# Kernel tuning notes

Hardware: AMD Instinct MI355X
Metric: run time of the kernel (lower is better)

The kernel has to match this reference:

```python
import jax, jax.numpy as jnp
import numpy as np

EPS_LN = 1e-5
EPS_BN = 1e-5


def ln_channels(x, w, b):
    # LayerNorm2d: normalize over channel dim of NCHW
    mu = x.mean(axis=1, keepdims=True)
    var = x.var(axis=1, keepdims=True)
    return (x - mu) / jnp.sqrt(var + EPS_LN) * w[None, :, None, None] + b[None, :, None, None]


def bn_eval(x, g, b):
    # eval-mode BatchNorm2d with running_mean=0, running_var=1
    return x / jnp.sqrt(1.0 + EPS_BN) * g[None, :, None, None] + b[None, :, None, None]


def conv1x1(x, w, b):
    return jnp.einsum('bchw,oc->bohw', x, w) + b[None, :, None, None]


def q_shift(x):
    # directional shift: 4 channel quarters shifted right/left/down/up by 1 px (zero pad)
    C = x.shape[1]
    q = C // 4
    return jnp.concatenate([
        jnp.pad(x[:, 0 * q:1 * q, :, :-1], ((0, 0), (0, 0), (0, 0), (1, 0))),
        jnp.pad(x[:, 1 * q:2 * q, :, 1:], ((0, 0), (0, 0), (0, 0), (0, 1))),
        jnp.pad(x[:, 2 * q:3 * q, :-1, :], ((0, 0), (0, 0), (1, 0), (0, 0))),
        jnp.pad(x[:, 3 * q:4 * q, 1:, :], ((0, 0), (0, 0), (0, 1), (0, 0))),
    ], axis=1)


def wkv_scan(k, v, w_neg, u):
    # numerically-stable RWKV WKV recurrence. k, v: [N, T, C]; w_neg (negative decay), u: [C]
    N, T, C = k.shape

    def step(carry, kv):
        a, b, p = carry
        kt, vt = kv
        q = jnp.maximum(p, u + kt)
        e1 = jnp.exp(p - q)
        e2 = jnp.exp(u + kt - q)
        out = (e1 * a + e2 * vt) / (e1 * b + e2)
        q2 = jnp.maximum(p + w_neg, kt)
        f1 = jnp.exp(p + w_neg - q2)
        f2 = jnp.exp(kt - q2)
        return (f1 * a + f2 * vt, f1 * b + f2, q2), out

    init = (jnp.zeros((N, C), k.dtype), jnp.zeros((N, C), k.dtype), jnp.full((N, C), -1e38, k.dtype))
    _, outs = jax.lax.scan(step, init, (jnp.swapaxes(k, 0, 1), jnp.swapaxes(v, 0, 1)))
    return jnp.swapaxes(outs, 0, 1)


def shape_guided_rwkv(x, mask, mix_k, mix_v, mix_r, Wk, Wv, Wr, Wo, decay, first, kn_w, kn_b):
    B, C, H, W = x.shape
    xs = q_shift(x)
    x_sh = mask * xs + (1.0 - mask) * x  # saliency-guided shift blend
    mk = mix_k[None, :, None, None]
    mv = mix_v[None, :, None, None]
    mr = mix_r[None, :, None, None]
    xk = x * mk + x_sh * (1.0 - mk)
    xv = x * mv + x_sh * (1.0 - mv)
    xr = x * mr + x_sh * (1.0 - mr)
    k = jnp.einsum('bchw,oc->bohw', xk, Wk)
    v = jnp.einsum('bchw,oc->bohw', xv, Wv)
    sr = jax.nn.sigmoid(jnp.einsum('bchw,oc->bohw', xr, Wr))
    w_neg = -jnp.exp(decay)
    # horizontal orientation: scan each row left->right
    kh = k.transpose(0, 2, 3, 1).reshape(B * H, W, C)
    vh = v.transpose(0, 2, 3, 1).reshape(B * H, W, C)
    wkv_h = wkv_scan(kh, vh, w_neg, first).reshape(B, H, W, C).transpose(0, 3, 1, 2)
    # vertical orientation: scan each column top->bottom
    kv_ = k.transpose(0, 3, 2, 1).reshape(B * W, H, C)
    vv_ = v.transpose(0, 3, 2, 1).reshape(B * W, H, C)
    wkv_v = wkv_scan(kv_, vv_, w_neg, first).reshape(B, W, H, C).transpose(0, 3, 2, 1)
    wkv = 0.5 * (wkv_h + wkv_v)
    wkv = ln_channels(wkv, kn_w, kn_b)  # key_norm=True
    out = jnp.einsum('bchw,oc->bohw', sr * wkv, Wo)
    return x + out


def channel_fusion(x, c1_w, c1_b, bn1_g, bn1_b, c2_w, c2_b, bn2_g, bn2_b, c3_w, c3_b, bn3_g, bn3_b):
    # grouped 3x3 conv (groups=2) -> GELU -> BN -> 1x1 expand -> GELU -> BN -> 1x1 reduce -> GELU -> BN
    y = jax.lax.conv_general_dilated(x, c1_w, (1, 1), 'SAME',
                                     dimension_numbers=('NCHW', 'OIHW', 'NCHW'),
                                     feature_group_count=2) + c1_b[None, :, None, None]
    y = bn_eval(jax.nn.gelu(y, approximate=False), bn1_g, bn1_b)
    y = bn_eval(jax.nn.gelu(conv1x1(y, c2_w, c2_b), approximate=False), bn2_g, bn2_b)
    y = bn_eval(jax.nn.gelu(conv1x1(y, c3_w, c3_b), approximate=False), bn3_g, bn3_b)
    return y


def patch_expand(x, up_w, up_b, s=2):
    B, C, H, W = x.shape
    y = conv1x1(x, up_w, up_b)  # [B, Cout*s*s, H, W]
    Cout = y.shape[1] // (s * s)
    y = y.reshape(B, Cout, s, s, H, W).transpose(0, 1, 4, 2, 5, 3).reshape(B, Cout, H * s, W * s)
    return y


def setup_inputs() -> dict:
    key = jax.random.key(0)
    B, C, Cs, Cout, H, W, s = 8, 256, 512, 128, 64, 64, 2
    ks = jax.random.split(key, 32)
    sc = C ** -0.5
    inp = {
        'x': jax.random.normal(ks[0], (B, C, H, W), jnp.float32),
        'skip': jax.random.normal(ks[1], (B, Cs, H, W), jnp.float32),
        'saliency_mask': jax.random.uniform(ks[2], (B, 1, H, W), jnp.float32),
        'ln1_w': jnp.ones((C,)), 'ln1_b': jnp.zeros((C,)),
        'ln2_w': jnp.ones((C,)), 'ln2_b': jnp.zeros((C,)),
        'mix_k': jax.random.uniform(ks[3], (C,)),
        'mix_v': jax.random.uniform(ks[4], (C,)),
        'mix_r': jax.random.uniform(ks[5], (C,)),
        'Wk': jax.random.normal(ks[6], (C, C)) * sc,
        'Wv': jax.random.normal(ks[7], (C, C)) * sc,
        'Wr': jax.random.normal(ks[8], (C, C)) * sc,
        'Wo': jax.random.normal(ks[9], (C, C)) * sc,
        'decay': jax.random.normal(ks[10], (C,)) * 0.5,
        'first': jax.random.normal(ks[11], (C,)) * 0.5,
        'kn_w': jnp.ones((C,)), 'kn_b': jnp.zeros((C,)),
        'sp_w': jax.random.normal(ks[12], (C, Cs)) * (Cs ** -0.5),
        'sp_b': jnp.zeros((C,)),
        'c1_w': jax.random.normal(ks[13], (2 * C, C, 3, 3)) * ((C * 9) ** -0.5),
        'c1_b': jnp.zeros((2 * C,)),
        'bn1_g': jnp.ones((2 * C,)), 'bn1_b': jnp.zeros((2 * C,)),
        'c2_w': jax.random.normal(ks[14], (4 * C, 2 * C)) * ((2 * C) ** -0.5),
        'c2_b': jnp.zeros((4 * C,)),
        'bn2_g': jnp.ones((4 * C,)), 'bn2_b': jnp.zeros((4 * C,)),
        'c3_w': jax.random.normal(ks[15], (C, 4 * C)) * ((4 * C) ** -0.5),
        'c3_b': jnp.zeros((C,)),
        'bn3_g': jnp.ones((C,)), 'bn3_b': jnp.zeros((C,)),
        'up_w': jax.random.normal(ks[16], (Cout * s * s, C)) * sc,
        'up_b': jnp.zeros((Cout * s * s,)),
    }
    return inp


def reference(x, skip, saliency_mask, ln1_w, ln1_b, ln2_w, ln2_b, mix_k, mix_v, mix_r,
              Wk, Wv, Wr, Wo, decay, first, kn_w, kn_b, sp_w, sp_b,
              c1_w, c1_b, bn1_g, bn1_b, c2_w, c2_b, bn2_g, bn2_b, c3_w, c3_b, bn3_g, bn3_b,
              up_w, up_b):
    xn = ln_channels(x, ln1_w, ln1_b)
    x_sg = shape_guided_rwkv(xn, saliency_mask, mix_k, mix_v, mix_r, Wk, Wv, Wr, Wo,
                             decay, first, kn_w, kn_b)
    skip_feat = conv1x1(skip, sp_w, sp_b)
    x_cat = jnp.concatenate([x_sg, skip_feat], axis=1)
    x_fused = channel_fusion(x_cat, c1_w, c1_b, bn1_g, bn1_b, c2_w, c2_b, bn2_g, bn2_b,
                             c3_w, c3_b, bn3_g, bn3_b)
    x_fused = ln_channels(x_fused, ln2_w, ln2_b)
    return patch_expand(x_fused, up_w, up_b, s=2)
```

## Files before the change

### kernel.cpp

```cpp
#include <hip/hip_runtime.h>
#include <hip/hip_bf16.h>
#include <math.h>

#define B_ 8
#define C_ 256
#define P_ 4096

typedef __bf16 bf16_t;
typedef __attribute__((ext_vector_type(8))) __bf16 bf16x8;
typedef __attribute__((ext_vector_type(4))) __bf16 bf16x4;
typedef __attribute__((ext_vector_type(4))) float f32x4;

template<typename T, int TRANS>
__global__ __launch_bounds__(256)
void ln_stats_kernel(const T* __restrict__ in, float2* __restrict__ stats)
{
    __shared__ float sred[4][64];
    __shared__ float s2red[4][64];
    int tid = threadIdx.x;
    if (TRANS) {
        int wp = tid >> 2, cw = tid & 3;
        int gp = blockIdx.x * 64 + wp;
        const bf16_t* row = (const bf16_t*)in + (size_t)gp * 256 + cw * 64;
        float s = 0.f, s2 = 0.f;
        #pragma unroll
        for (int i = 0; i < 64; i += 8) {
            bf16x8 v = *reinterpret_cast<const bf16x8*>(&row[i]);
            #pragma unroll
            for (int j = 0; j < 8; ++j) {
                float f = (float)v[j]; s += f; s2 += f * f;
            }
        }
        sred[cw][wp] = s; s2red[cw][wp] = s2;
        __syncthreads();
        if (cw == 0) {
            s  = sred[0][wp]  + sred[1][wp]  + sred[2][wp]  + sred[3][wp];
            s2 = s2red[0][wp] + s2red[1][wp] + s2red[2][wp] + s2red[3][wp];
            float mu  = s * (1.f / 256.f);
            float var = s2 * (1.f / 256.f) - mu * mu;
            stats[gp] = make_float2(mu, 1.0f / sqrtf(var + 1e-5f));
        }
        return;
    }
    int wp = tid & 63, cw = tid >> 6;
    int gp = blockIdx.x * 64 + wp;
    int b  = gp >> 12, p = gp & 4095;
    size_t base = (size_t)b * 256 * 4096 + p;
    float s = 0.f, s2 = 0.f;
    #pragma unroll 8
    for (int cc = 0; cc < 64; ++cc) {
        float v = (float)in[base + (size_t)(cw * 64 + cc) * 4096];
        s += v; s2 += v * v;
    }
    sred[cw][wp] = s; s2red[cw][wp] = s2;
    __syncthreads();
    if (cw == 0) {
        s  = sred[0][wp]  + sred[1][wp]  + sred[2][wp]  + sred[3][wp];
        s2 = s2red[0][wp] + s2red[1][wp] + s2red[2][wp] + s2red[3][wp];
        float mu  = s * (1.f / 256.f);
        float var = s2 * (1.f / 256.f) - mu * mu;
        stats[gp] = make_float2(mu, 1.0f / sqrtf(var + 1e-5f));
    }
}

__global__ __launch_bounds__(256)
void skip_transpose_kernel(const float* __restrict__ in, bf16_t* __restrict__ outT)
{
    __shared__ bf16_t t[64 * 66];
    int p0 = blockIdx.x << 6;
    int c0 = blockIdx.y << 6;
    int b  = blockIdx.z;
    int tid = threadIdx.x;
    int pl = tid & 63, cq = tid >> 6;
    const float* src = in + ((size_t)b * 512 + c0) * 4096 + p0;
    #pragma unroll
    for (int i = 0; i < 16; ++i) {
        int cl = i * 4 + cq;
        t[pl * 66 + cl] = (bf16_t)src[(size_t)cl * 4096 + pl];
    }
    __syncthreads();
    int pw = tid >> 2, ch = tid & 3;
    bf16x8 v0 = *reinterpret_cast<const bf16x8*>(&t[pw * 66 + ch * 16]);
    bf16x8 v1 = *reinterpret_cast<const bf16x8*>(&t[pw * 66 + ch * 16 + 8]);
    bf16_t* dst = outT + ((size_t)b * 4096 + p0 + pw) * 512 + c0 + ch * 16;
    *reinterpret_cast<bf16x8*>(dst) = v0;
    *reinterpret_cast<bf16x8*>(dst + 8) = v1;
}

__global__ __launch_bounds__(256)
void qshift_mix_kernel(const float* __restrict__ x, const float2* __restrict__ st1,
                       const float* __restrict__ mask,
                       const float* __restrict__ gw, const float* __restrict__ gb,
                       const float* __restrict__ mk_, const float* __restrict__ mv_,
                       const float* __restrict__ mr_,
                       bf16_t* __restrict__ xk, bf16_t* __restrict__ xv,
                       bf16_t* __restrict__ xr)
{
    int gid = blockIdx.x * 256 + threadIdx.x;
    int g = gid << 3;
    int p = g & 4095;
    int c = (g >> 12) & 255;
    int b = g >> 20;
    int h = p >> 6, w0 = p & 63;
    float gwc = gw[c], gbc = gb[c];
    int sbase = (b << 12) + p;

    float4 x0 = *reinterpret_cast<const float4*>(&x[g]);
    float4 x1 = *reinterpret_cast<const float4*>(&x[g + 4]);
    float xv8[8] = {x0.x, x0.y, x0.z, x0.w, x1.x, x1.y, x1.z, x1.w};
    float2 s8[8];
    #pragma unroll
    for (int i = 0; i < 4; ++i) {
        float4 t = *reinterpret_cast<const float4*>(&st1[sbase + i * 2]);
        s8[2 * i]     = make_float2(t.x, t.y);
        s8[2 * i + 1] = make_float2(t.z, t.w);
    }
    float xn8[8];
    #pragma unroll
    for (int i = 0; i < 8; ++i)
        xn8[i] = (xv8[i] - s8[i].x) * s8[i].y * gwc + gbc;

    float xs8[8];
    int quad = c >> 6;
    if (quad == 0) {
        xs8[0] = 0.f;
        if (w0 > 0) {
            float xm = x[g - 1]; float2 sm = st1[sbase - 1];
            xs8[0] = (xm - sm.x) * sm.y * gwc + gbc;
        }
        #pragma unroll
        for (int i = 1; i < 8; ++i) xs8[i] = xn8[i - 1];
    } else if (quad == 1) {
        #pragma unroll
        for (int i = 0; i < 7; ++i) xs8[i] = xn8[i + 1];
        xs8[7] = 0.f;
        if (w0 + 8 < 64) {
            float xp = x[g + 8]; float2 sp = st1[sbase + 8];
            xs8[7] = (xp - sp.x) * sp.y * gwc + gbc;
        }
    } else {
        int d = (quad == 2) ? -64 : 64;
        bool ok = (quad == 2) ? (h > 0) : (h < 63);
        if (ok) {
            float4 y0 = *reinterpret_cast<const float4*>(&x[g + d]);
            float4 y1 = *reinterpret_cast<const float4*>(&x[g + d + 4]);
            float yv8[8] = {y0.x, y0.y, y0.z, y0.w, y1.x, y1.y, y1.z, y1.w};
            #pragma unroll
            for (int i = 0; i < 4; ++i) {
                float4 t = *reinterpret_cast<const float4*>(&st1[sbase + d + i * 2]);
                float2 sa = make_float2(t.x, t.y), sb = make_float2(t.z, t.w);
                xs8[2 * i]     = (yv8[2 * i]     - sa.x) * sa.y * gwc + gbc;
                xs8[2 * i + 1] = (yv8[2 * i + 1] - sb.x) * sb.y * gwc + gbc;
            }
        } else {
            #pragma unroll
            for (int i = 0; i < 8; ++i) xs8[i] = 0.f;
        }
    }

    float4 m0 = *reinterpret_cast<const float4*>(&mask[sbase]);
    float4 m1 = *reinterpret_cast<const float4*>(&mask[sbase + 4]);
    float mm[8] = {m0.x, m0.y, m0.z, m0.w, m1.x, m1.y, m1.z, m1.w};
    float xsh8[8];
    #pragma unroll
    for (int i = 0; i < 8; ++i)
        xsh8[i] = mm[i] * xs8[i] + (1.f - mm[i]) * xn8[i];

    float ak = mk_[c], av = mv_[c], ar = mr_[c];
    bf16x8 ok_, ov_, or_;
    #pragma unroll
    for (int i = 0; i < 8; ++i) {
        ok_[i] = (bf16_t)(ak * xn8[i] + (1.f - ak) * xsh8[i]);
        ov_[i] = (bf16_t)(av * xn8[i] + (1.f - av) * xsh8[i]);
        or_[i] = (bf16_t)(ar * xn8[i] + (1.f - ar) * xsh8[i]);
    }
    *reinterpret_cast<bf16x8*>(&xk[g]) = ok_;
    *reinterpret_cast<bf16x8*>(&xv[g]) = ov_;
    *reinterpret_cast<bf16x8*>(&xr[g]) = or_;
}

#define EP_NONE    0
#define EP_SIGMOID 1
#define EP_BIAS    2
#define EP_RESLN   3
#define EP_GELU_BN 4
#define EP_SHUFFLE 5
#define EP_KVR     6
#define EP_WOSKIP  7

template<int NB, int BMODE, int EPI, int OUTBF, int TILE, int OTR>
__global__ __launch_bounds__(256, (TILE == 64) ? 4 : 2)
void mfma_gemm(const bf16_t* __restrict__ Wp, const void* __restrict__ Xin,
               const bf16_t* __restrict__ X2,
               const float2* __restrict__ bstats, const float* __restrict__ blnw,
               const float* __restrict__ blnb,
               const float* __restrict__ bias, const bf16_t* __restrict__ skipT,
               const float* __restrict__ bng, const float* __restrict__ bnb,
               const float* __restrict__ resx, const float2* __restrict__ estats,
               const float* __restrict__ elnw, const float* __restrict__ elnb,
               void* __restrict__ OutV,
               int O, int K, int Cstride, int obs, int ocoff)
{
    constexpr int MI = TILE / 32;
    constexpr int BROWS = (NB == 3) ? 2 * 66 : TILE;
    __shared__ bf16_t Alds[NB * TILE * 36];
    __shared__ bf16_t Blds[BROWS * 36];
    int tid = threadIdx.x;
    int bx = blockIdx.x;
    int o0 = blockIdx.y * TILE;
    int b  = blockIdx.z;
    int p0 = bx * TILE;
    int cbase = (NB == 3) ? ((o0 >> 8) << 8) : 0;

    bool wo = true;
    int bb = b;
    if (EPI == EP_WOSKIP) { wo = (b >> 3) != 0; bb = b & 7; }

    const bf16_t* Wpe = Wp;
    if (EPI == EP_KVR)    Wpe = Wp + (size_t)(b >> 3) * O * K;
    if (EPI == EP_WOSKIP) Wpe = wo ? Wp : (Wp + 65536);
    int Krun = K;
    if (EPI == EP_WOSKIP) Krun = wo ? 256 : 512;

    int lane = tid & 63, wid = tid >> 6;
    int l15 = lane & 15;
    int lk8 = (lane >> 4) << 3;
    int mbase = (wid >> 1) * (TILE / 2);
    int nbase = (wid & 1) * (TILE / 2);

    const bf16_t* Xb_bf = (const bf16_t*)Xin + (size_t)bb * Cstride * 4096;
    const float*  Xb_f  = (const float*)Xin + (size_t)bb * Cstride * 4096;
    const bf16_t* X2b   = (BMODE == 3) ? X2 + (size_t)bb * Cstride * 4096 : nullptr;
    const bf16_t* skb   = (EPI == EP_WOSKIP)
                          ? skipT + (size_t)bb * 4096 * 512 : nullptr;

    f32x4 acc[MI][MI] = {};

    if (NB == 3 && tid < 144) {
        int r = tid / 72, rest = tid % 72;
        int col = rest / 36, cc = rest % 36;
        Blds[(r * 66 + (col ? 65 : 0)) * 36 + cc] = (bf16_t)0.f;
    }

    for (int kh = 0; kh < NB; ++kh) {
        for (int c0 = 0; c0 < Krun; c0 += 32) {
            __syncthreads();
            if (NB == 3) {
                #pragma unroll
                for (int q = 0; q < 2; ++q) {
                    int cid = tid + q * 256;
                    int r   = cid >> 8;
                    int w   = (cid >> 2) & 63;
                    int ch4 = cid & 3;
                    int hr  = (bx << 1) + kh - 1 + r;
                    bf16x8 bv;
                    #pragma unroll
                    for (int i = 0; i < 8; ++i) bv[i] = (bf16_t)0.f;
                    if (hr >= 0 && hr < 64)
                        bv = *reinterpret_cast<const bf16x8*>(
                               Xb_bf + (size_t)((hr << 6) + w) * 512
                                     + cbase + c0 + ch4 * 8);
                    *reinterpret_cast<bf16x8*>(
                        &Blds[(r * 66 + w + 1) * 36 + ch4 * 8]) = bv;
                }
            } else if (BMODE >= 4) {
                constexpr int NCH = (TILE == 128) ? 2 : 1;
                #pragma unroll
                for (int q = 0; q < NCH; ++q) {
                    int cid = tid + q * 256;
                    int p   = cid >> 2;
                    int ch4 = cid & 3;
                    bf16x8 bv = *reinterpret_cast<const bf16x8*>(
                        Xb_bf + (size_t)(p0 + p) * Cstride + c0 + ch4 * 8);
                    if (BMODE == 5) {
                        float2 st = bstats[(bb << 12) + p0 + p];
                        #pragma unroll
                        for (int j = 0; j < 8; ++j) {
                            int cc = c0 + ch4 * 8 + j;
                            bv[j] = (bf16_t)(((float)bv[j] - st.x) * st.y
                                             * blnw[cc] + blnb[cc]);
                        }
                    }
                    *reinterpret_cast<bf16x8*>(&Blds[p * 36 + ch4 * 8]) = bv;
                }
            } else if (EPI == EP_WOSKIP && !wo) {
                int p = tid >> 2, ch4 = tid & 3;
                bf16x8 bv = *reinterpret_cast<const bf16x8*>(
                    skb + (size_t)(p0 + p) * 512 + c0 + ch4 * 8);
                *reinterpret_cast<bf16x8*>(&Blds[p * 36 + ch4 * 8]) = bv;
            } else {
                int p_loc = tid & (TILE - 1);
                float2 st = make_float2(0.f, 1.f);
                if (BMODE == 3)
                    st = bstats[(bb << 12) + p0 + p_loc];
                #pragma unroll
                for (int rep = 0; rep < (TILE == 128 ? 2 : 1); ++rep) {
                    int cgr = (TILE == 128) ? ((tid >> 7) + rep * 2) : (tid >> 6);
                    bf16x8 bv;
                    size_t gbase = (size_t)(c0 + cgr * 8) * 4096 + p0 + p_loc;
                    #pragma unroll
                    for (int j = 0; j < 8; ++j) {
                        size_t gi = gbase + (size_t)j * 4096;
                        int cc = c0 + cgr * 8 + j;
                        if (BMODE == 0) {
                            bv[j] = Xb_bf[gi];
                        } else {
                            float v = ((float)Xb_bf[gi] - st.x) * st.y * blnw[cc] + blnb[cc];
                            if (BMODE == 3) v *= (float)X2b[gi];
                            bv[j] = (bf16_t)v;
                        }
                    }
                    *reinterpret_cast<bf16x8*>(&Blds[p_loc * 36 + cgr * 8]) = bv;
                }
            }
            if (TILE == 128) {
                int ao = tid >> 1, aq = tid & 1;
                #pragma unroll
                for (int t = 0; t < NB; ++t) {
                    const bf16_t* wsrc = (NB == 3)
                        ? Wpe + ((size_t)(kh * 3 + t) * O + o0 + ao) * 256 + c0
                        : Wpe + (size_t)(o0 + ao) * Krun + c0;
                    bf16x8 w0 = *reinterpret_cast<const bf16x8*>(wsrc + aq * 8);
                    bf16x8 w1 = *reinterpret_cast<const bf16x8*>(wsrc + (aq + 2) * 8);
                    *reinterpret_cast<bf16x8*>(&Alds[(t * 128 + ao) * 36 + aq * 8]) = w0;
                    *reinterpret_cast<bf16x8*>(&Alds[(t * 128 + ao) * 36 + (aq + 2) * 8]) = w1;
                }
            } else {
                int ao = tid >> 2, aq = tid & 3;
                const bf16_t* wsrc = Wpe + (size_t)(o0 + ao) * Krun + c0;
                bf16x8 w0 = *reinterpret_cast<const bf16x8*>(wsrc + aq * 8);
                *reinterpret_cast<bf16x8*>(&Alds[ao * 36 + aq * 8]) = w0;
            }
            __syncthreads();
            #pragma unroll
            for (int t = 0; t < NB; ++t) {
                bf16x8 af[MI];
                #pragma unroll
                for (int i = 0; i < MI; ++i)
                    af[i] = *reinterpret_cast<const bf16x8*>(
                              &Alds[(t * TILE + mbase + i * 16 + l15) * 36 + lk8]);
                #pragma unroll
                for (int j = 0; j < MI; ++j) {
                    int pl = nbase + j * 16;
                    int baddr;
                    if (NB == 3)
                        baddr = ((pl >> 6) * 66 + (pl & 63) + l15 + t) * 36 + lk8;
                    else
                        baddr = (pl + l15) * 36 + lk8;
                    bf16x8 bfv = *reinterpret_cast<const bf16x8*>(&Blds[baddr]);
                    #pragma unroll
                    for (int i = 0; i < MI; ++i)
                        acc[i][j] = __builtin_amdgcn_mfma_f32_16x16x32_bf16(
                                        af[i], bfv, acc[i][j], 0, 0, 0);
                }
            }
        }
    }

    const float bnsc = 1.0f / sqrtf(1.f + 1e-5f);
    bool kvr_sig = (EPI == EP_KVR) && (b >= 16);

    if (EPI == EP_WOSKIP) {
        int oco = wo ? 0 : 256;
        #pragma unroll
        for (int i = 0; i < MI; ++i) {
            int ob = o0 + mbase + i * 16 + ((lane >> 4) << 2);
            float bi4[4], rw4[4], rb4[4];
            #pragma unroll
            for (int r = 0; r < 4; ++r) {
                bi4[r] = wo ? 0.f : bias[ob + r];
                rw4[r] = wo ? elnw[ob + r] : 0.f;
                rb4[r] = wo ? elnb[ob + r] : 0.f;
            }
            #pragma unroll
            for (int j = 0; j < MI; ++j) {
                int pp = p0 + nbase + j * 16 + l15;
                float2 st = make_float2(0.f, 1.f);
                if (wo) st = estats[(bb << 12) + pp];
                bf16x4 pk;
                #pragma unroll
                for (int r = 0; r < 4; ++r) {
                    float t = acc[i][j][r];
                    if (!wo) {
                        t += bi4[r];
                    } else {
                        float rv = resx[((size_t)bb * 256 + ob + r) * 4096 + pp];
                        t += (rv - st.x) * st.y * rw4[r] + rb4[r];
                    }
                    pk[r] = (bf16_t)t;
                }
                *reinterpret_cast<bf16x4*>(
                    &((bf16_t*)OutV)[((size_t)bb * 4096 + pp) * 512 + oco + ob]) = pk;
            }
        }
        return;
    }

    if (EPI == EP_GELU_BN && OTR) {
        #pragma unroll
        for (int i = 0; i < MI; ++i) {
            int ob = o0 + mbase + i * 16 + ((lane >> 4) << 2);
            float bi4[4], sc4[4], sh4[4];
            #pragma unroll
            for (int r = 0; r < 4; ++r) {
                bi4[r] = bias[ob + r];
                sc4[r] = bng[ob + r] * bnsc;
                sh4[r] = bnb[ob + r];
            }
            #pragma unroll
            for (int j = 0; j < MI; ++j) {
                int pp = p0 + nbase + j * 16 + l15;
                bf16x4 pk;
                #pragma unroll
                for (int r = 0; r < 4; ++r) {
                    float t = acc[i][j][r] + bi4[r];
                    t = 0.5f * t * (1.f + erff(t * 0.70710678118654752f));
                    pk[r] = (bf16_t)(t * sc4[r] + sh4[r]);
                }
                *reinterpret_cast<bf16x4*>(
                    &((bf16_t*)OutV)[((size_t)bb * 4096 + pp) * obs + ocoff + ob]) = pk;
            }
        }
        return;
    }

    #pragma unroll
    for (int i = 0; i < MI; ++i) {
        #pragma unroll
        for (int r = 0; r < 4; ++r) {
            int o = o0 + mbase + i * 16 + ((lane >> 4) << 2) + r;
            float bi = 0.f;
            if (EPI == EP_BIAS || EPI == EP_GELU_BN || EPI == EP_SHUFFLE) bi = bias[o];
            float sc = 0.f, sh = 0.f;
            if (EPI == EP_GELU_BN) { sc = bng[o] * bnsc; sh = bnb[o]; }
            float rw = 0.f, rb = 0.f;
            if (EPI == EP_RESLN) { rw = elnw[o]; rb = elnb[o]; }
            #pragma unroll
            for (int j = 0; j < MI; ++j) {
                int pp = p0 + nbase + j * 16 + l15;
                float t = acc[i][j][r];
                if (EPI == EP_SIGMOID) t = 1.f / (1.f + expf(-t));
                if (EPI == EP_KVR && kvr_sig) t = 1.f / (1.f + expf(-t));
                if (EPI == EP_BIAS || EPI == EP_GELU_BN || EPI == EP_SHUFFLE) t += bi;
                if (EPI == EP_RESLN) {
                    float2 st = estats[(bb << 12) + pp];
                    float rv = resx[((size_t)bb * 256 + o) * 4096 + pp];
                    t += (rv - st.x) * st.y * rw + rb;
                }
                if (EPI == EP_GELU_BN) {
                    t = 0.5f * t * (1.f + erff(t * 0.70710678118654752f));
                    t = t * sc + sh;
                }
                if (EPI == EP_SHUFFLE) {
                    int co = o >> 2, s1 = (o >> 1) & 1, s2 = o & 1;
                    int hh = pp >> 6, ww = pp & 63;
                    ((float*)OutV)[(((size_t)bb * 128 + co) * 128 + hh * 2 + s1) * 128
                                   + ww * 2 + s2] = t;
                } else {
                    size_t oidx = ((size_t)bb * obs + ocoff + o) * 4096 + pp;
                    if (OUTBF) ((bf16_t*)OutV)[oidx] = (bf16_t)t;
                    else       ((float*)OutV)[oidx]  = t;
                }
            }
        }
    }
}

__global__ __launch_bounds__(256)
void pack_all_kernel(const float* __restrict__ wk, const float* __restrict__ wv,
                     const float* __restrict__ wr, const float* __restrict__ wo,
                     const float* __restrict__ sp, const float* __restrict__ c2,
                     const float* __restrict__ c3, const float* __restrict__ up,
                     const float* __restrict__ c1, bf16_t* __restrict__ outfl,
                     bf16_t* __restrict__ outc1)
{
    int g = blockIdx.x * 256 + threadIdx.x;
    if (g < 1310720) {
        float v;
        if      (g < 65536)   v = wk[g];
        else if (g < 131072)  v = wv[g - 65536];
        else if (g < 196608)  v = wr[g - 131072];
        else if (g < 262144)  v = wo[g - 196608];
        else if (g < 393216)  v = sp[g - 262144];
        else if (g < 917504)  v = c2[g - 393216];
        else if (g < 1179648) v = c3[g - 917504];
        else                  v = up[g - 1179648];
        outfl[g] = (bf16_t)v;
    } else {
        int g2 = g - 1310720;
        if (g2 < 1179648) {
            int c = g2 & 255;
            int o = (g2 >> 8) & 511;
            int tap = g2 >> 17;
            outc1[g2] = (bf16_t)c1[(size_t)o * 2304 + c * 9 + tap];
        }
    }
}

__global__ __launch_bounds__(64)
void wkv_h_kernel(const bf16_t* __restrict__ kin, const bf16_t* __restrict__ vin,
                  bf16_t* __restrict__ outw,
                  const float* __restrict__ decay, const float* __restrict__ first)
{
    __shared__ bf16_t ks[64 * 66];
    __shared__ bf16_t vs[64 * 66];
    int c0 = blockIdx.x * 64;
    int h  = blockIdx.y;
    int b  = blockIdx.z;
    int tid = threadIdx.x;
    size_t base = (((size_t)b * 256 + c0) * 64 + h) * 64;

    for (int f = tid; f < 64 * 64; f += 64) {
        int cc = f >> 6, w = f & 63;
        ks[cc * 66 + w] = kin[base + (size_t)cc * 4096 + w];
        vs[cc * 66 + w] = vin[base + (size_t)cc * 4096 + w];
    }
    __syncthreads();

    int c = c0 + tid;
    float u  = first[c];
    float wn = -expf(decay[c]);
    float a = 0.f, bb = 0.f, pp = -1e38f;
    for (int t = 0; t < 64; ++t) {
        float kt = (float)ks[tid * 66 + t], vt = (float)vs[tid * 66 + t];
        float q  = fmaxf(pp, u + kt);
        float e1 = expf(pp - q), e2 = expf(u + kt - q);
        float ov = (e1 * a + e2 * vt) / (e1 * bb + e2);
        ks[tid * 66 + t] = (bf16_t)ov;
        float q2 = fmaxf(pp + wn, kt);
        float f1 = expf(pp + wn - q2), f2 = expf(kt - q2);
        a = f1 * a + f2 * vt;
        bb = f1 * bb + f2;
        pp = q2;
    }
    __syncthreads();
    for (int f = tid; f < 64 * 64; f += 64) {
        int cc = f >> 6, w = f & 63;
        outw[base + (size_t)cc * 4096 + w] = ks[cc * 66 + w];
    }
}

__global__ __launch_bounds__(256)
void wkv_v_kernel(const bf16_t* __restrict__ kin, const bf16_t* __restrict__ vin,
                  bf16_t* __restrict__ outw,
                  const float* __restrict__ decay, const float* __restrict__ first)
{
    int g = blockIdx.x * 256 + threadIdx.x;
    int w = g & 63;
    int c = (g >> 6) & 255;
    int b = g >> 14;
    size_t base = (size_t)(b * 256 + c) * 4096 + w;
    float u  = first[c];
    float wn = -expf(decay[c]);
    float a = 0.f, bb = 0.f, pp = -1e38f;
    for (int h = 0; h < 64; ++h) {
        size_t idx = base + h * 64;
        float kt = (float)kin[idx], vt = (float)vin[idx];
        float q  = fmaxf(pp, u + kt);
        float e1 = expf(pp - q), e2 = expf(u + kt - q);
        float ov = (e1 * a + e2 * vt) / (e1 * bb + e2);
        outw[idx] = (bf16_t)(0.5f * ((float)outw[idx] + ov));
        float q2 = fmaxf(pp + wn, kt);
        float f1 = expf(pp + wn - q2), f2 = expf(kt - q2);
        a = f1 * a + f2 * vt;
        bb = f1 * bb + f2;
        pp = q2;
    }
}

extern "C" void kernel_launch(void* const* d_in, const int* in_sizes, int n_in,
                              void* d_out, int out_size, void* d_ws, size_t ws_size,
                              hipStream_t stream)
{
    const float* x      = (const float*)d_in[0];
    const float* skip   = (const float*)d_in[1];
    const float* mask   = (const float*)d_in[2];
    const float* ln1_w  = (const float*)d_in[3];
    const float* ln1_b  = (const float*)d_in[4];
    const float* ln2_w  = (const float*)d_in[5];
    const float* ln2_b  = (const float*)d_in[6];
    const float* mix_k  = (const float*)d_in[7];
    const float* mix_v  = (const float*)d_in[8];
    const float* mix_r  = (const float*)d_in[9];
    const float* Wk     = (const float*)d_in[10];
    const float* Wv     = (const float*)d_in[11];
    const float* Wr     = (const float*)d_in[12];
    const float* Wo     = (const float*)d_in[13];
    const float* decay  = (const float*)d_in[14];
    const float* first  = (const float*)d_in[15];
    const float* kn_w   = (const float*)d_in[16];
    const float* kn_b   = (const float*)d_in[17];
    const float* sp_w   = (const float*)d_in[18];
    const float* sp_b   = (const float*)d_in[19];
    const float* c1_w   = (const float*)d_in[20];
    const float* c1_b   = (const float*)d_in[21];
    const float* bn1_g  = (const float*)d_in[22];
    const float* bn1_b  = (const float*)d_in[23];
    const float* c2_w   = (const float*)d_in[24];
    const float* c2_b   = (const float*)d_in[25];
    const float* bn2_g  = (const float*)d_in[26];
    const float* bn2_b  = (const float*)d_in[27];
    const float* c3_w   = (const float*)d_in[28];
    const float* c3_b   = (const float*)d_in[29];
    const float* bn3_g  = (const float*)d_in[30];
    const float* bn3_b  = (const float*)d_in[31];
    const float* up_w   = (const float*)d_in[32];
    const float* up_b   = (const float*)d_in[33];
    float* out = (float*)d_out;

    float* ws = (float*)d_ws;
    const size_t S = 8388608;
    const size_t Hs = S / 2;
    bf16_t* xk   = (bf16_t*)ws;
    bf16_t* xv   = (bf16_t*)(ws + Hs);
    bf16_t* xr   = (bf16_t*)(ws + 2 * Hs);
    bf16_t* kbuf = (bf16_t*)(ws + 3 * Hs);
    bf16_t* vbuf = (bf16_t*)(ws + 4 * Hs);
    bf16_t* rbuf = (bf16_t*)(ws + 5 * Hs);
    bf16_t* wkv  = (bf16_t*)(ws + 6 * Hs);
    bf16_t* xcat = (bf16_t*)(ws + 7 * Hs);
    bf16_t* skbf = (bf16_t*)(ws + 9 * Hs);
    bf16_t* y1   = (bf16_t*)(ws + 9 * Hs);
    bf16_t* y2   = (bf16_t*)ws;
    bf16_t* y3   = (bf16_t*)(ws + 4 * Hs);
    float*  wtop = ws + 11 * Hs;
    bf16_t* w9   = (bf16_t*)wtop;
    bf16_t* wfl  = w9 + 1179648;
    float2* st1  = (float2*)(wfl + 1310720);
    float2* stk  = st1 + 32768;
    float2* st2  = stk + 32768;
    bf16_t* wkb = wfl;
    bf16_t* wob = wfl + 196608;
    bf16_t* c2b = wfl + 393216;
    bf16_t* c3b = wfl + 917504;
    bf16_t* upb = wfl + 1179648;

    dim3 blk(256);

    pack_all_kernel<<<dim3(9728), blk, 0, stream>>>(Wk, Wv, Wr, Wo, sp_w, c2_w,
                                                    c3_w, up_w, c1_w, wfl, w9);
    ln_stats_kernel<float, 0><<<dim3(512), blk, 0, stream>>>(x, st1);
    skip_transpose_kernel<<<dim3(64, 8, 8), blk, 0, stream>>>(skip, skbf);

    qshift_mix_kernel<<<dim3(4096), blk, 0, stream>>>(x, st1, mask, ln1_w, ln1_b,
                                                      mix_k, mix_v, mix_r, xk, xv, xr);
    mfma_gemm<1, 0, EP_KVR, 1, 64, 0><<<dim3(64, 4, 24), blk, 0, stream>>>(
        wkb, xk, nullptr, nullptr, nullptr, nullptr, nullptr, nullptr, nullptr,
        nullptr, nullptr, nullptr, nullptr, nullptr, kbuf, 256, 256, 256, 256, 0);
    wkv_h_kernel<<<dim3(4, 64, 8), dim3(64), 0, stream>>>(kbuf, vbuf, wkv, decay, first);
    wkv_v_kernel<<<dim3(512), blk, 0, stream>>>(kbuf, vbuf, wkv, decay, first);
    ln_stats_kernel<bf16_t, 0><<<dim3(512), blk, 0, stream>>>(wkv, stk);
    mfma_gemm<1, 3, EP_WOSKIP, 1, 64, 0><<<dim3(64, 4, 16), blk, 0, stream>>>(
        wob, wkv, rbuf, stk, kn_w, kn_b, sp_b, skbf, nullptr, nullptr,
        x, st1, ln1_w, ln1_b, xcat, 256, 0, 256, 512, 0);
    mfma_gemm<3, 0, EP_GELU_BN, 1, 128, 1><<<dim3(32, 4, 8), blk, 0, stream>>>(
        w9, xcat, nullptr, nullptr, nullptr, nullptr, c1_b, nullptr, bn1_g, bn1_b,
        nullptr, nullptr, nullptr, nullptr, y1, 512, 256, 512, 512, 0);
    mfma_gemm<1, 4, EP_GELU_BN, 1, 128, 1><<<dim3(32, 8, 8), blk, 0, stream>>>(
        c2b, y1, nullptr, nullptr, nullptr, nullptr, c2_b, nullptr, bn2_g, bn2_b,
        nullptr, nullptr, nullptr, nullptr, y2, 1024, 512, 512, 1024, 0);
    mfma_gemm<1, 4, EP_GELU_BN, 1, 64, 1><<<dim3(64, 4, 8), blk, 0, stream>>>(
        c3b, y2, nullptr, nullptr, nullptr, nullptr, c3_b, nullptr, bn3_g, bn3_b,
        nullptr, nullptr, nullptr, nullptr, y3, 256, 1024, 1024, 256, 0);
    ln_stats_kernel<bf16_t, 1><<<dim3(512), blk, 0, stream>>>(y3, st2);
    mfma_gemm<1, 5, EP_SHUFFLE, 0, 64, 0><<<dim3(64, 8, 8), blk, 0, stream>>>(
        upb, y3, nullptr, st2, ln2_w, ln2_b, up_b, nullptr, nullptr, nullptr,
        nullptr, nullptr, nullptr, nullptr, out, 512, 256, 256, 0, 0);
}
```

Baseline: 468.8 us.

## Merge WKV scans into one kernel and feed Wo GEMM transposed inputs

The two WKV passes (horizontal and vertical) now run in a single kernel. Each block holds one full 64x64 channel plane of k and v in LDS, so k/v are read once and the intermediate output is not written to and re-read from global memory. The LN-stats kernel also writes a pixel-major bf16 copy of the WKV output, and the KVR GEMM writes the sigmoid r output pixel-major. This lets the Wo GEMM load its B operand with vectorized contiguous loads instead of strided per-channel gathers. The costs are an extra transposed write in the stats pass and only 64-thread blocks carrying a serial scan in the merged kernel.

```diff
diff --git a/kernel.cpp b/kernel.cpp
--- a/kernel.cpp
+++ b/kernel.cpp
@@ -11,9 +11,10 @@
 typedef __attribute__((ext_vector_type(4))) __bf16 bf16x4;
 typedef __attribute__((ext_vector_type(4))) float f32x4;
 
-template<typename T, int TRANS>
+template<typename T, int TRANS, int TROUT>
 __global__ __launch_bounds__(256)
-void ln_stats_kernel(const T* __restrict__ in, float2* __restrict__ stats)
+void ln_stats_kernel(const T* __restrict__ in, float2* __restrict__ stats,
+                     bf16_t* __restrict__ outT)
 {
     __shared__ float sred[4][64];
     __shared__ float s2red[4][64];
@@ -47,10 +48,17 @@
     int b  = gp >> 12, p = gp & 4095;
     size_t base = (size_t)b * 256 * 4096 + p;
     float s = 0.f, s2 = 0.f;
+    bf16x8 chunk;
     #pragma unroll 8
     for (int cc = 0; cc < 64; ++cc) {
         float v = (float)in[base + (size_t)(cw * 64 + cc) * 4096];
         s += v; s2 += v * v;
+        if (TROUT) {
+            chunk[cc & 7] = (bf16_t)v;
+            if ((cc & 7) == 7)
+                *reinterpret_cast<bf16x8*>(
+                    &outT[(size_t)gp * 256 + cw * 64 + (cc & ~7)]) = chunk;
+        }
     }
     sred[cw][wp] = s; s2red[cw][wp] = s2;
     __syncthreads();
@@ -283,16 +291,30 @@
                     }
                     *reinterpret_cast<bf16x8*>(&Blds[p * 36 + ch4 * 8]) = bv;
                 }
-            } else if (EPI == EP_WOSKIP && !wo) {
+            } else if (EPI == EP_WOSKIP) {
                 int p = tid >> 2, ch4 = tid & 3;
-                bf16x8 bv = *reinterpret_cast<const bf16x8*>(
-                    skb + (size_t)(p0 + p) * 512 + c0 + ch4 * 8);
-                *reinterpret_cast<bf16x8*>(&Blds[p * 36 + ch4 * 8]) = bv;
+                if (!wo) {
+                    bf16x8 bv = *reinterpret_cast<const bf16x8*>(
+                        skb + (size_t)(p0 + p) * 512 + c0 + ch4 * 8);
+                    *reinterpret_cast<bf16x8*>(&Blds[p * 36 + ch4 * 8]) = bv;
+                } else {
+                    bf16x8 wv = *reinterpret_cast<const bf16x8*>(
+                        Xb_bf + (size_t)(p0 + p) * 256 + c0 + ch4 * 8);
+                    bf16x8 rv = *reinterpret_cast<const bf16x8*>(
+                        X2b + (size_t)(p0 + p) * 256 + c0 + ch4 * 8);
+                    float2 st = bstats[(bb << 12) + p0 + p];
+                    bf16x8 bv;
+                    #pragma unroll
+                    for (int j = 0; j < 8; ++j) {
+                        int cc = c0 + ch4 * 8 + j;
+                        float v = ((float)wv[j] - st.x) * st.y * blnw[cc] + blnb[cc];
+                        v *= (float)rv[j];
+                        bv[j] = (bf16_t)v;
+                    }
+                    *reinterpret_cast<bf16x8*>(&Blds[p * 36 + ch4 * 8]) = bv;
+                }
             } else {
                 int p_loc = tid & (TILE - 1);
-                float2 st = make_float2(0.f, 1.f);
-                if (BMODE == 3)
-                    st = bstats[(bb << 12) + p0 + p_loc];
                 #pragma unroll
                 for (int rep = 0; rep < (TILE == 128 ? 2 : 1); ++rep) {
                     int cgr = (TILE == 128) ? ((tid >> 7) + rep * 2) : (tid >> 6);
@@ -301,14 +323,8 @@
                     #pragma unroll
                     for (int j = 0; j < 8; ++j) {
                         size_t gi = gbase + (size_t)j * 4096;
-                        int cc = c0 + cgr * 8 + j;
-                        if (BMODE == 0) {
-                            bv[j] = Xb_bf[gi];
-                        } else {
-                            float v = ((float)Xb_bf[gi] - st.x) * st.y * blnw[cc] + blnb[cc];
-                            if (BMODE == 3) v *= (float)X2b[gi];
-                            bv[j] = (bf16_t)v;
-                        }
+                        if (BMODE == 0) bv[j] = Xb_bf[gi];
+                        else            bv[j] = (bf16_t)Xb_f[gi];
                     }
                     *reinterpret_cast<bf16x8*>(&Blds[p_loc * 36 + cgr * 8]) = bv;
                 }
@@ -358,7 +374,27 @@
     }
 
     const float bnsc = 1.0f / sqrtf(1.f + 1e-5f);
-    bool kvr_sig = (EPI == EP_KVR) && (b >= 16);
+
+    if (EPI == EP_KVR && b >= 16) {
+        bf16_t* rT = (bf16_t*)OutV + (size_t)16 * 256 * 4096;
+        #pragma unroll
+        for (int i = 0; i < MI; ++i) {
+            int ob = o0 + mbase + i * 16 + ((lane >> 4) << 2);
+            #pragma unroll
+            for (int j = 0; j < MI; ++j) {
+                int pp = p0 + nbase + j * 16 + l15;
+                bf16x4 pk;
+                #pragma unroll
+                for (int r = 0; r < 4; ++r) {
+                    float t = acc[i][j][r];
+                    pk[r] = (bf16_t)(1.f / (1.f + expf(-t)));
+                }
+                *reinterpret_cast<bf16x4*>(
+                    &rT[((size_t)(b - 16) * 4096 + pp) * 256 + ob]) = pk;
+            }
+        }
+        return;
+    }
 
     if (EPI == EP_WOSKIP) {
         int oco = wo ? 0 : 256;
@@ -433,20 +469,12 @@
             if (EPI == EP_BIAS || EPI == EP_GELU_BN || EPI == EP_SHUFFLE) bi = bias[o];
             float sc = 0.f, sh = 0.f;
             if (EPI == EP_GELU_BN) { sc = bng[o] * bnsc; sh = bnb[o]; }
-            float rw = 0.f, rb = 0.f;
-            if (EPI == EP_RESLN) { rw = elnw[o]; rb = elnb[o]; }
             #pragma unroll
             for (int j = 0; j < MI; ++j) {
                 int pp = p0 + nbase + j * 16 + l15;
                 float t = acc[i][j][r];
                 if (EPI == EP_SIGMOID) t = 1.f / (1.f + expf(-t));
-                if (EPI == EP_KVR && kvr_sig) t = 1.f / (1.f + expf(-t));
                 if (EPI == EP_BIAS || EPI == EP_GELU_BN || EPI == EP_SHUFFLE) t += bi;
-                if (EPI == EP_RESLN) {
-                    float2 st = estats[(bb << 12) + pp];
-                    float rv = resx[((size_t)bb * 256 + o) * 4096 + pp];
-                    t += (rv - st.x) * st.y * rw + rb;
-                }
                 if (EPI == EP_GELU_BN) {
                     t = 0.5f * t * (1.f + erff(t * 0.70710678118654752f));
                     t = t * sc + sh;
@@ -498,73 +526,86 @@
 }
 
 __global__ __launch_bounds__(64)
-void wkv_h_kernel(const bf16_t* __restrict__ kin, const bf16_t* __restrict__ vin,
-                  bf16_t* __restrict__ outw,
-                  const float* __restrict__ decay, const float* __restrict__ first)
+void wkv_merged_kernel(const bf16_t* __restrict__ kin, const bf16_t* __restrict__ vin,
+                       bf16_t* __restrict__ outw,
+                       const float* __restrict__ decay, const float* __restrict__ first)
 {
     __shared__ bf16_t ks[64 * 66];
     __shared__ bf16_t vs[64 * 66];
-    int c0 = blockIdx.x * 64;
-    int h  = blockIdx.y;
-    int b  = blockIdx.z;
+    __shared__ bf16_t os[64 * 66];
+    int c = blockIdx.x;
+    int b = blockIdx.y;
     int tid = threadIdx.x;
-    size_t base = (((size_t)b * 256 + c0) * 64 + h) * 64;
-
-    for (int f = tid; f < 64 * 64; f += 64) {
-        int cc = f >> 6, w = f & 63;
-        ks[cc * 66 + w] = kin[base + (size_t)cc * 4096 + w];
-        vs[cc * 66 + w] = vin[base + (size_t)cc * 4096 + w];
+    size_t base = ((size_t)b * 256 + c) * 4096;
+
+    uint32_t* ksu = (uint32_t*)ks;
+    uint32_t* vsu = (uint32_t*)vs;
+    uint32_t* osu = (uint32_t*)os;
+    #pragma unroll
+    for (int i = 0; i < 8; ++i) {
+        int idx = i * 512 + tid * 8;
+        int row = idx >> 6, col = idx & 63;
+        bf16x8 kv = *reinterpret_cast<const bf16x8*>(&kin[base + idx]);
+        bf16x8 vv = *reinterpret_cast<const bf16x8*>(&vin[base + idx]);
+        uint32_t* kp = (uint32_t*)&kv;
+        uint32_t* vp = (uint32_t*)&vv;
+        #pragma unroll
+        for (int q = 0; q < 4; ++q) {
+            ksu[row * 33 + (col >> 1) + q] = kp[q];
+            vsu[row * 33 + (col >> 1) + q] = vp[q];
+        }
     }
     __syncthreads();
 
-    int c = c0 + tid;
     float u  = first[c];
     float wn = -expf(decay[c]);
-    float a = 0.f, bb = 0.f, pp = -1e38f;
-    for (int t = 0; t < 64; ++t) {
-        float kt = (float)ks[tid * 66 + t], vt = (float)vs[tid * 66 + t];
-        float q  = fmaxf(pp, u + kt);
-        float e1 = expf(pp - q), e2 = expf(u + kt - q);
-        float ov = (e1 * a + e2 * vt) / (e1 * bb + e2);
-        ks[tid * 66 + t] = (bf16_t)ov;
-        float q2 = fmaxf(pp + wn, kt);
-        float f1 = expf(pp + wn - q2), f2 = expf(kt - q2);
-        a = f1 * a + f2 * vt;
-        bb = f1 * bb + f2;
-        pp = q2;
+
+    {
+        int h = tid;
+        float a = 0.f, bb2 = 0.f, pp = -1e38f;
+        for (int w = 0; w < 64; ++w) {
+            float kt = (float)ks[h * 66 + w], vt = (float)vs[h * 66 + w];
+            float q  = fmaxf(pp, u + kt);
+            float e1 = expf(pp - q), e2 = expf(u + kt - q);
+            float ov = (e1 * a + e2 * vt) / (e1 * bb2 + e2);
+            os[h * 66 + w] = (bf16_t)ov;
+            float q2 = fmaxf(pp + wn, kt);
+            float f1 = expf(pp + wn - q2), f2 = expf(kt - q2);
+            a = f1 * a + f2 * vt;
+            bb2 = f1 * bb2 + f2;
+            pp = q2;
+        }
     }
     __syncthreads();
-    for (int f = tid; f < 64 * 64; f += 64) {
-        int cc = f >> 6, w = f & 63;
-        outw[base + (size_t)cc * 4096 + w] = ks[cc * 66 + w];
-    }
-}
-
-__global__ __launch_bounds__(256)
-void wkv_v_kernel(const bf16_t* __restrict__ kin, const bf16_t* __restrict__ vin,
-                  bf16_t* __restrict__ outw,
-                  const float* __restrict__ decay, const float* __restrict__ first)
-{
-    int g = blockIdx.x * 256 + threadIdx.x;
-    int w = g & 63;
-    int c = (g >> 6) & 255;
-    int b = g >> 14;
-    size_t base = (size_t)(b * 256 + c) * 4096 + w;
-    float u  = first[c];
-    float wn = -expf(decay[c]);
-    float a = 0.f, bb = 0.f, pp = -1e38f;
-    for (int h = 0; h < 64; ++h) {
-        size_t idx = base + h * 64;
-        float kt = (float)kin[idx], vt = (float)vin[idx];
-        float q  = fmaxf(pp, u + kt);
-        float e1 = expf(pp - q), e2 = expf(u + kt - q);
-        float ov = (e1 * a + e2 * vt) / (e1 * bb + e2);
-        outw[idx] = (bf16_t)(0.5f * ((float)outw[idx] + ov));
-        float q2 = fmaxf(pp + wn, kt);
-        float f1 = expf(pp + wn - q2), f2 = expf(kt - q2);
-        a = f1 * a + f2 * vt;
-        bb = f1 * bb + f2;
-        pp = q2;
+
+    {
+        int w = tid;
+        float a = 0.f, bb2 = 0.f, pp = -1e38f;
+        for (int h = 0; h < 64; ++h) {
+            float kt = (float)ks[h * 66 + w], vt = (float)vs[h * 66 + w];
+            float q  = fmaxf(pp, u + kt);
+            float e1 = expf(pp - q), e2 = expf(u + kt - q);
+            float ov = (e1 * a + e2 * vt) / (e1 * bb2 + e2);
+            os[h * 66 + w] = (bf16_t)(0.5f * ((float)os[h * 66 + w] + ov));
+            float q2 = fmaxf(pp + wn, kt);
+            float f1 = expf(pp + wn - q2), f2 = expf(kt - q2);
+            a = f1 * a + f2 * vt;
+            bb2 = f1 * bb2 + f2;
+            pp = q2;
+        }
+    }
+    __syncthreads();
+
+    #pragma unroll
+    for (int i = 0; i < 8; ++i) {
+        int idx = i * 512 + tid * 8;
+        int row = idx >> 6, col = idx & 63;
+        bf16x8 ov;
+        uint32_t* op = (uint32_t*)&ov;
+        #pragma unroll
+        for (int q = 0; q < 4; ++q)
+            op[q] = osu[row * 33 + (col >> 1) + q];
+        *reinterpret_cast<bf16x8*>(&outw[base + idx]) = ov;
     }
 }
 
@@ -614,6 +655,7 @@
     bf16_t* xk   = (bf16_t*)ws;
     bf16_t* xv   = (bf16_t*)(ws + Hs);
     bf16_t* xr   = (bf16_t*)(ws + 2 * Hs);
+    bf16_t* wkvT = (bf16_t*)(ws + 2 * Hs);
     bf16_t* kbuf = (bf16_t*)(ws + 3 * Hs);
     bf16_t* vbuf = (bf16_t*)(ws + 4 * Hs);
     bf16_t* rbuf = (bf16_t*)(ws + 5 * Hs);
@@ -639,7 +681,7 @@
 
     pack_all_kernel<<<dim3(9728), blk, 0, stream>>>(Wk, Wv, Wr, Wo, sp_w, c2_w,
                                                     c3_w, up_w, c1_w, wfl, w9);
-    ln_stats_kernel<float, 0><<<dim3(512), blk, 0, stream>>>(x, st1);
+    ln_stats_kernel<float, 0, 0><<<dim3(512), blk, 0, stream>>>(x, st1, nullptr);
     skip_transpose_kernel<<<dim3(64, 8, 8), blk, 0, stream>>>(skip, skbf);
 
     qshift_mix_kernel<<<dim3(4096), blk, 0, stream>>>(x, st1, mask, ln1_w, ln1_b,
@@ -647,11 +689,10 @@
     mfma_gemm<1, 0, EP_KVR, 1, 64, 0><<<dim3(64, 4, 24), blk, 0, stream>>>(
         wkb, xk, nullptr, nullptr, nullptr, nullptr, nullptr, nullptr, nullptr,
         nullptr, nullptr, nullptr, nullptr, nullptr, kbuf, 256, 256, 256, 256, 0);
-    wkv_h_kernel<<<dim3(4, 64, 8), dim3(64), 0, stream>>>(kbuf, vbuf, wkv, decay, first);
-    wkv_v_kernel<<<dim3(512), blk, 0, stream>>>(kbuf, vbuf, wkv, decay, first);
-    ln_stats_kernel<bf16_t, 0><<<dim3(512), blk, 0, stream>>>(wkv, stk);
+    wkv_merged_kernel<<<dim3(256, 8), dim3(64), 0, stream>>>(kbuf, vbuf, wkv, decay, first);
+    ln_stats_kernel<bf16_t, 0, 1><<<dim3(512), blk, 0, stream>>>(wkv, stk, wkvT);
     mfma_gemm<1, 3, EP_WOSKIP, 1, 64, 0><<<dim3(64, 4, 16), blk, 0, stream>>>(
-        wob, wkv, rbuf, stk, kn_w, kn_b, sp_b, skbf, nullptr, nullptr,
+        wob, wkvT, rbuf, stk, kn_w, kn_b, sp_b, skbf, nullptr, nullptr,
         x, st1, ln1_w, ln1_b, xcat, 256, 0, 256, 512, 0);
     mfma_gemm<3, 0, EP_GELU_BN, 1, 128, 1><<<dim3(32, 4, 8), blk, 0, stream>>>(
         w9, xcat, nullptr, nullptr, nullptr, nullptr, c1_b, nullptr, bn1_g, bn1_b,
@@ -662,7 +703,7 @@
     mfma_gemm<1, 4, EP_GELU_BN, 1, 64, 1><<<dim3(64, 4, 8), blk, 0, stream>>>(
         c3b, y2, nullptr, nullptr, nullptr, nullptr, c3_b, nullptr, bn3_g, bn3_b,
         nullptr, nullptr, nullptr, nullptr, y3, 256, 1024, 1024, 256, 0);
-    ln_stats_kernel<bf16_t, 1><<<dim3(512), blk, 0, stream>>>(y3, st2);
+    ln_stats_kernel<bf16_t, 1, 0><<<dim3(512), blk, 0, stream>>>(y3, st2, nullptr);
     mfma_gemm<1, 5, EP_SHUFFLE, 0, 64, 0><<<dim3(64, 8, 8), blk, 0, stream>>>(
         upb, y3, nullptr, st2, ln2_w, ln2_b, up_b, nullptr, nullptr, nullptr,
         nullptr, nullptr, nullptr, nullptr, out, 512, 256, 256, 0, 0);
```

Result: no change. 474.5 us (+1.2%).
